# Performance work log

Hardware: AMD Instinct MI355X
Metric: run time of the kernel (lower is better)

Reference implementation:

```python
import jax, jax.numpy as jnp
import numpy as np

ND, NC = 100000, 20000
E_DD, E_DC, E_CD = 1600000, 800000, 800000
DDIM, CDIM, H, B = 256, 512, 128, 100000


def _lin_init(k, out_d, in_d):
    kw, kb = jax.random.split(k)
    s = 1.0 / np.sqrt(in_d)
    return (jax.random.uniform(kw, (out_d, in_d), jnp.float32, -s, s),
            jax.random.uniform(kb, (out_d,), jnp.float32, -s, s))


def setup_inputs() -> dict:
    key = jax.random.key(0)
    ks = jax.random.split(key, 32)
    inp = {
        'x_drug': jax.random.normal(ks[0], (ND, DDIM), jnp.float32),
        'x_cell': jax.random.normal(ks[1], (NC, CDIM), jnp.float32),
        'ei_dd_src': jax.random.randint(ks[2], (E_DD,), 0, ND),
        'ei_dd_dst': jax.random.randint(ks[3], (E_DD,), 0, ND),
        'ei_dc_src': jax.random.randint(ks[4], (E_DC,), 0, ND),
        'ei_dc_dst': jax.random.randint(ks[5], (E_DC,), 0, NC),
        'ei_cd_src': jax.random.randint(ks[6], (E_CD,), 0, NC),
        'ei_cd_dst': jax.random.randint(ks[7], (E_CD,), 0, ND),
        'q_da': jax.random.randint(ks[8], (B,), 0, ND),
        'q_db': jax.random.randint(ks[9], (B,), 0, ND),
        'q_c': jax.random.randint(ks[10], (B,), 0, NC),
    }
    # input projections
    inp['wd'], inp['bd'] = _lin_init(ks[11], H, DDIM)
    inp['wc'], inp['bc'] = _lin_init(ks[12], H, CDIM)
    # per-edge-type SAGEConv params: lin_l (W+b, on aggregated neighbors), lin_r (W only, on root)
    i = 13
    for name in ['dd1', 'cd1', 'dc1', 'dd2', 'cd2', 'dc2']:
        wl, bl = _lin_init(ks[i], H, H)
        wr, _ = _lin_init(ks[i + 1], H, H)
        inp[name + '_wl'], inp[name + '_bl'], inp[name + '_wr'] = wl, bl, wr
        i += 2
    # MLP head
    inp['m1_w'], inp['m1_b'] = _lin_init(ks[i], H, 3 * H)
    inp['m2_w'], inp['m2_b'] = _lin_init(ks[i + 1], 1, H)
    return inp


def _sage(x_src, x_dst, src, dst, wl, bl, wr):
    # SAGEConv: mean-aggregate neighbor (src) features onto dst, then lin_l + lin_r(root)
    n_dst = x_dst.shape[0]
    agg = jax.ops.segment_sum(x_src[src], dst, num_segments=n_dst)  # [n_dst, H]
    cnt = jax.ops.segment_sum(jnp.ones(src.shape, x_src.dtype), dst, num_segments=n_dst)
    mean = agg / jnp.maximum(cnt, 1.0)[:, None]
    return mean @ wl.T + bl + x_dst @ wr.T


def reference(x_drug, x_cell, wd, bd, wc, bc,
              dd1_wl, dd1_bl, dd1_wr, cd1_wl, cd1_bl, cd1_wr, dc1_wl, dc1_bl, dc1_wr,
              dd2_wl, dd2_bl, dd2_wr, cd2_wl, cd2_bl, cd2_wr, dc2_wl, dc2_bl, dc2_wr,
              m1_w, m1_b, m2_w, m2_b,
              ei_dd_src, ei_dd_dst, ei_dc_src, ei_dc_dst, ei_cd_src, ei_cd_dst,
              q_da, q_db, q_c):
    xd = x_drug @ wd.T + bd  # [ND, H]
    xc = x_cell @ wc.T + bc  # [NC, H]
    # layer 1 (to_hetero: sum contributions per dst node type, then relu)
    hd = jax.nn.relu(_sage(xd, xd, ei_dd_src, ei_dd_dst, dd1_wl, dd1_bl, dd1_wr)
                     + _sage(xc, xd, ei_cd_src, ei_cd_dst, cd1_wl, cd1_bl, cd1_wr))
    hc = jax.nn.relu(_sage(xd, xc, ei_dc_src, ei_dc_dst, dc1_wl, dc1_bl, dc1_wr))
    # layer 2 (no activation)
    od = (_sage(hd, hd, ei_dd_src, ei_dd_dst, dd2_wl, dd2_bl, dd2_wr)
          + _sage(hc, hd, ei_cd_src, ei_cd_dst, cd2_wl, cd2_bl, cd2_wr))
    oc = _sage(hd, hc, ei_dc_src, ei_dc_dst, dc2_wl, dc2_bl, dc2_wr)
    combined = jnp.concatenate([od[q_da], od[q_db], oc[q_c]], axis=-1)  # [B, 3H]
    h = jax.nn.relu(combined @ m1_w.T + m1_b)  # dropout is eval-mode identity
    return (h @ m2_w.T + m2_b)[:, 0]
```

## Files before the change

kernel.cpp:

```cpp
#include <hip/hip_runtime.h>
#include <hip/hip_fp16.h>

typedef _Float16 f16;
typedef f16 f16x8 __attribute__((ext_vector_type(8)));
typedef float f32x4 __attribute__((ext_vector_type(4)));

#define NDRUG 100000
#define NCELL 20000
#define EDD   1600000
#define EDC   800000
#define ECD   800000
#define NQ    100000
#define ETOT  (EDD + ECD + EDC)
#define CAP_DD 64
#define CAP_CD 64
#define CAP_DC 128

#define NBD 782
#define NBC 313
#define NBTOT (NBD + NBC)
#define ECHUNK 4096
#define NBLK ((ETOT + ECHUNK - 1) / ECHUNK)
#define BCAP 6144

__device__ inline int bucket_of(int rdst) { return rdst < 200000 ? (rdst >> 8) : NBD + ((rdst - 200000) >> 6); }
__device__ inline int dl_of(int rdst)     { return rdst < 200000 ? (rdst & 255) : ((rdst - 200000) & 63); }

__device__ inline int rdst_decode(int e, const int* __restrict__ ddd,
                                  const int* __restrict__ cdd, const int* __restrict__ dcd)
{
    if (e < EDD) return ddd[e];
    if (e < EDD + ECD) return 100000 + cdd[e - EDD];
    return 200000 + dcd[e - EDD - ECD];
}


__global__ __launch_bounds__(256) void hist_k(const int* __restrict__ ddd, const int* __restrict__ cdd,
                                              const int* __restrict__ dcd, int* __restrict__ bucket_tot)
{
    __shared__ int lh[NBTOT];
    for (int i = threadIdx.x; i < NBTOT; i += 256) lh[i] = 0;
    __syncthreads();
    int base = blockIdx.x * ECHUNK;
    for (int j = threadIdx.x; j < ECHUNK; j += 256) {
        int e = base + j;
        if (e < ETOT) atomicAdd(&lh[bucket_of(rdst_decode(e, ddd, cdd, dcd))], 1);
    }
    __syncthreads();
    for (int i = threadIdx.x; i < NBTOT; i += 256) {
        int c = lh[i];
        if (c) atomicAdd(&bucket_tot[i], c);
    }
}


__global__ __launch_bounds__(256) void scanbase_k(const int* __restrict__ tot,
                                                  int* __restrict__ basearr, int* __restrict__ cur)
{
    __shared__ int vals[1280];
    __shared__ int seg[256];
    int tid = threadIdx.x;
    for (int i = tid; i < 1280; i += 256) vals[i] = (i < NBTOT) ? tot[i] : 0;
    __syncthreads();
    int mine[5]; int s = 0;
#pragma unroll
    for (int j = 0; j < 5; ++j) { mine[j] = vals[tid * 5 + j]; s += mine[j]; }
    seg[tid] = s; __syncthreads();
    for (int o = 1; o < 256; o <<= 1) {
        int v = (tid >= o) ? seg[tid - o] : 0;
        __syncthreads();
        seg[tid] += v;
        __syncthreads();
    }
    int base = seg[tid] - s;
#pragma unroll
    for (int j = 0; j < 5; ++j) {
        int idx = tid * 5 + j;
        if (idx < NBTOT) { basearr[idx] = base; cur[idx] = base; }
        base += mine[j];
    }
}


__global__ __launch_bounds__(256) void scatter_k(
    const int* __restrict__ dds, const int* __restrict__ ddd,
    const int* __restrict__ cds, const int* __restrict__ cdd,
    const int* __restrict__ dcs, const int* __restrict__ dcd,
    int* __restrict__ bucket_cur, unsigned* __restrict__ binned)
{
    __shared__ int lh[NBTOT];
    __shared__ int lbase[NBTOT];
    __shared__ unsigned lrec[ECHUNK];
    __shared__ unsigned short lbkt[ECHUNK];
    for (int i = threadIdx.x; i < NBTOT; i += 256) lh[i] = 0;
    __syncthreads();
    int base = blockIdx.x * ECHUNK;
    for (int j = threadIdx.x; j < ECHUNK; j += 256) {
        int e = base + j;
        if (e < ETOT) {
            int src, rdst;
            if (e < EDD) { src = dds[e]; rdst = ddd[e]; }
            else if (e < EDD + ECD) { int i2 = e - EDD; src = cds[i2]; rdst = 100000 + cdd[i2]; }
            else { int i2 = e - EDD - ECD; src = dcs[i2]; rdst = 200000 + dcd[i2]; }
            int b = bucket_of(rdst);
            lrec[j] = ((unsigned)dl_of(rdst) << 17) | (unsigned)src;
            lbkt[j] = (unsigned short)b;
            atomicAdd(&lh[b], 1);
        } else {
            lbkt[j] = 0xFFFFu;
        }
    }
    __syncthreads();
    for (int i = threadIdx.x; i < NBTOT; i += 256) {
        int c = lh[i];
        lbase[i] = c ? atomicAdd(&bucket_cur[i], c) : 0;
        lh[i] = 0;
    }
    __syncthreads();
    for (int j = threadIdx.x; j < ECHUNK; j += 256) {
        unsigned short b = lbkt[j];
        if (b != 0xFFFFu) {
            int r = atomicAdd(&lh[b], 1);
            binned[lbase[b] + r] = lrec[j];
        }
    }
}


__global__ __launch_bounds__(256) void bucket_build_k(
    const unsigned* __restrict__ binned, const int* __restrict__ bucket_base, const int* __restrict__ bucket_tot,
    int* __restrict__ cnt_dd, int* __restrict__ cnt_cd, int* __restrict__ cnt_dc,
    int* __restrict__ l_dd, int* __restrict__ l_cd, int* __restrict__ l_dc)
{
    __shared__ unsigned recs[BCAP];
    __shared__ int cnt[256];
    __shared__ int off[256];
    __shared__ int cur[256];
    __shared__ int seg[256];

    int b = blockIdx.x, tid = threadIdx.x;
    int tot = bucket_tot[b];
    int base = bucket_base[b];
    int n = tot < BCAP ? tot : BCAP;

    cnt[tid] = 0;
    __syncthreads();
    for (int j = tid; j < n; j += 256) {
        unsigned r = binned[base + j];
        recs[j] = r;
        atomicAdd(&cnt[r >> 17], 1);
    }
    __syncthreads();
    int c = cnt[tid];
    seg[tid] = c; __syncthreads();
    for (int o = 1; o < 256; o <<= 1) {
        int v = (tid >= o) ? seg[tid - o] : 0;
        __syncthreads();
        seg[tid] += v;
        __syncthreads();
    }
    int ex = seg[tid] - c;
    off[tid] = ex; cur[tid] = ex;
    __syncthreads();

    for (int j = tid; j < n; j += 256) {
        unsigned r = recs[j];
        int dl = r >> 17;
        int src = r & 0x1FFFF;
        int rank = atomicAdd(&cur[dl], 1) - off[dl];
        if (b < NBD) {
            int rdst = b * 256 + dl;
            if (rdst < 100000) { if (rank < CAP_DD) l_dd[(size_t)rdst * CAP_DD + rank] = src; }
            else               { if (rank < CAP_CD) l_cd[(size_t)(rdst - 100000) * CAP_CD + rank] = src; }
        } else {
            int node = (b - NBD) * 64 + dl;
            if (rank < CAP_DC) l_dc[(size_t)node * CAP_DC + rank] = src;
        }
    }

    if (b < NBD) {
        int rdst = b * 256 + tid;
        if (rdst < 200000) {
            if (rdst < 100000) cnt_dd[rdst] = cnt[tid];
            else               cnt_cd[rdst - 100000] = cnt[tid];
        }
    } else {
        if (tid < 64) {
            int node = (b - NBD) * 64 + tid;
            if (node < NCELL) cnt_dc[node] = cnt[tid];
        }
    }
}


__device__ inline void addv(float* acc, uint4 v)
{
    const __half2* h = (const __half2*)&v;
#pragma unroll
    for (int j = 0; j < 4; ++j) {
        float2 f = __half22float2(h[j]);
        acc[2 * j]     += f.x;
        acc[2 * j + 1] += f.y;
    }
}

__global__ __launch_bounds__(256) void agg_all_k(
    const __half* __restrict__ t_d, const __half* __restrict__ t_c,
    const int* __restrict__ cnt_dd, const int* __restrict__ cnt_cd, const int* __restrict__ cnt_dc,
    const int* __restrict__ l_dd, const int* __restrict__ l_cd, const int* __restrict__ l_dc,
    __half* __restrict__ m_a, __half* __restrict__ m_b, __half* __restrict__ m_c)
{
    int node = blockIdx.x * 16 + (threadIdx.x >> 4);
    int g = threadIdx.x & 15;

    const int* list; int n; const __half* tab; __half* out;
    if (node < NDRUG) {
        list = l_dd + (size_t)node * CAP_DD; n = cnt_dd[node];
        if (n > CAP_DD) n = CAP_DD;
        tab = t_d; out = m_a + (size_t)node * 128;
    } else if (node < 2 * NDRUG) {
        int m = node - NDRUG;
        list = l_cd + (size_t)m * CAP_CD; n = cnt_cd[m];
        if (n > CAP_CD) n = CAP_CD;
        tab = t_c; out = m_b + (size_t)m * 128;
    } else if (node < 2 * NDRUG + NCELL) {
        int m = node - 2 * NDRUG;
        list = l_dc + (size_t)m * CAP_DC; n = cnt_dc[m];
        if (n > CAP_DC) n = CAP_DC;
        tab = t_d; out = m_c + (size_t)m * 128;
    } else return;

    const __half* base = tab + (size_t)g * 8;

    float acc[8];
#pragma unroll
    for (int j = 0; j < 8; ++j) acc[j] = 0.f;

    int i = 0;
    for (; i + 3 < n; i += 4) {
        int s0 = list[i], s1 = list[i + 1], s2 = list[i + 2], s3 = list[i + 3];
        uint4 v0 = *(const uint4*)(base + (size_t)s0 * 128);
        uint4 v1 = *(const uint4*)(base + (size_t)s1 * 128);
        uint4 v2 = *(const uint4*)(base + (size_t)s2 * 128);
        uint4 v3 = *(const uint4*)(base + (size_t)s3 * 128);
        addv(acc, v0); addv(acc, v1); addv(acc, v2); addv(acc, v3);
    }
    for (; i < n; ++i) {
        uint4 v = *(const uint4*)(base + (size_t)list[i] * 128);
        addv(acc, v);
    }

    float inv = 1.f / fmaxf((float)n, 1.f);
    __half h[8];
#pragma unroll
    for (int j = 0; j < 8; ++j) h[j] = __float2half(acc[j] * inv);
    *(uint4*)(out + g * 8) = *(uint4*)h;
}


__global__ __launch_bounds__(256) void prep_k(
    const float* __restrict__ wd,     const float* __restrict__ wc,     const float* __restrict__ m1w,
    const float* __restrict__ dd1_wl, const float* __restrict__ cd1_wl, const float* __restrict__ dc1_wl,
    const float* __restrict__ dc1_wr, const float* __restrict__ dd1_wr, const float* __restrict__ cd1_wr,
    const float* __restrict__ dd1_bl, const float* __restrict__ cd1_bl,
    const float* __restrict__ dd2_wl, const float* __restrict__ cd2_wl, const float* __restrict__ dc2_wl,
    const float* __restrict__ dc2_wr, const float* __restrict__ dd2_wr, const float* __restrict__ cd2_wr,
    const float* __restrict__ dd2_bl, const float* __restrict__ cd2_bl,
    f16* __restrict__ wd16, f16* __restrict__ wc16, f16* __restrict__ m1w16,
    f16* __restrict__ dd1_wl16, f16* __restrict__ cd1_wl16, f16* __restrict__ dc1_wl16,
    f16* __restrict__ dc1_wr16, f16* __restrict__ wr1s16,
    f16* __restrict__ dd2_wl16, f16* __restrict__ cd2_wl16, f16* __restrict__ dc2_wl16,
    f16* __restrict__ dc2_wr16, f16* __restrict__ wr2s16,
    float* __restrict__ bsum1, float* __restrict__ bsum2)
{
    int i = blockIdx.x * 256 + threadIdx.x;
    if (i < 128 * 256) wd16[i] = (f16)wd[i];
    if (i < 128 * 512) wc16[i] = (f16)wc[i];
    if (i < 128 * 384) m1w16[i] = (f16)m1w[i];
    if (i < 128 * 128) {
        dd1_wl16[i] = (f16)dd1_wl[i];
        cd1_wl16[i] = (f16)cd1_wl[i];
        dc1_wl16[i] = (f16)dc1_wl[i];
        dc1_wr16[i] = (f16)dc1_wr[i];
        wr1s16[i]   = (f16)(dd1_wr[i] + cd1_wr[i]);
        dd2_wl16[i] = (f16)dd2_wl[i];
        cd2_wl16[i] = (f16)cd2_wl[i];
        dc2_wl16[i] = (f16)dc2_wl[i];
        dc2_wr16[i] = (f16)dc2_wr[i];
        wr2s16[i]   = (f16)(dd2_wr[i] + cd2_wr[i]);
    }
    if (i < 128) {
        bsum1[i] = dd1_bl[i] + cd1_bl[i];
        bsum2[i] = dd2_bl[i] + cd2_bl[i];
    }
}


template<typename AT, int MODE>
__global__ __launch_bounds__(256) void mgemm_k(
    const AT* __restrict__ A0, const int* __restrict__ I0, const f16* __restrict__ W0, int K0, int S0,
    const AT* __restrict__ A1, const int* __restrict__ I1, const f16* __restrict__ W1, int K1, int S1,
    const AT* __restrict__ A2, const int* __restrict__ I2, const f16* __restrict__ W2, int K2, int S2,
    const float* __restrict__ bias, const float* __restrict__ m2w, const float* __restrict__ m2b,
    f16* __restrict__ Ch, float* __restrict__ Cf, int M)
{
    __shared__ f16 As[128][72];
    __shared__ f16 Ws[128][72];

    const int tid = threadIdx.x;
    const int w  = tid >> 6;
    const int l  = tid & 63;
    const int lc = l & 15;
    const int lq = l >> 4;
    const int mb = blockIdx.x * 128;
    const int sr = tid >> 1;
    const int sk = (tid & 1) * 32;

    f32x4 acc[2][8];
#pragma unroll
    for (int mi = 0; mi < 2; ++mi)
#pragma unroll
        for (int j = 0; j < 8; ++j) acc[mi][j] = (f32x4){0.f, 0.f, 0.f, 0.f};

    const AT*  Aseg[3] = {A0, A1, A2};
    const int* Iseg[3] = {I0, I1, I2};
    const f16* Wseg[3] = {W0, W1, W2};
    const int  Kseg[3] = {K0, K1, K2};
    const int  Sseg[3] = {S0, S1, S2};

    for (int s = 0; s < 3; ++s) {
        const AT* A = Aseg[s];
        if (!A) continue;
        const int* idx = Iseg[s];
        const f16* W = Wseg[s];
        const int K = Kseg[s], S = Sseg[s];

        int m = mb + sr; if (m >= M) m = M - 1;
        const AT*  arow = A + (size_t)(idx ? idx[m] : m) * (size_t)K;
        const f16* wrow = W + (size_t)sr * (size_t)S;

        for (int kt = 0; kt < K; kt += 64) {
            if constexpr (sizeof(AT) == 2) {
                const uint4* ap = (const uint4*)(arow + kt + sk);
                uint4 a0 = ap[0], a1 = ap[1], a2 = ap[2], a3 = ap[3];
                *(uint4*)&As[sr][sk]      = a0;
                *(uint4*)&As[sr][sk + 8]  = a1;
                *(uint4*)&As[sr][sk + 16] = a2;
                *(uint4*)&As[sr][sk + 24] = a3;
            } else {
                const float4* ap = (const float4*)(arow + kt + sk);
#pragma unroll
                for (int i = 0; i < 4; ++i) {
                    float4 u = ap[2 * i], v = ap[2 * i + 1];
                    f16x8 h;
                    h[0] = (f16)u.x; h[1] = (f16)u.y; h[2] = (f16)u.z; h[3] = (f16)u.w;
                    h[4] = (f16)v.x; h[5] = (f16)v.y; h[6] = (f16)v.z; h[7] = (f16)v.w;
                    *(f16x8*)&As[sr][sk + 8 * i] = h;
                }
            }
            {
                const uint4* wp = (const uint4*)(wrow + kt + sk);
                uint4 w0 = wp[0], w1 = wp[1], w2 = wp[2], w3 = wp[3];
                *(uint4*)&Ws[sr][sk]      = w0;
                *(uint4*)&Ws[sr][sk + 8]  = w1;
                *(uint4*)&Ws[sr][sk + 16] = w2;
                *(uint4*)&Ws[sr][sk + 24] = w3;
            }
            __syncthreads();

#pragma unroll
            for (int ks = 0; ks < 64; ks += 32) {
                f16x8 a0 = *(const f16x8*)&As[32 * w + lc][ks + 8 * lq];
                f16x8 a1 = *(const f16x8*)&As[32 * w + 16 + lc][ks + 8 * lq];
#pragma unroll
                for (int j = 0; j < 8; ++j) {
                    f16x8 b = *(const f16x8*)&Ws[16 * j + lc][ks + 8 * lq];
                    acc[0][j] = __builtin_amdgcn_mfma_f32_16x16x32_f16(a0, b, acc[0][j], 0, 0, 0);
                    acc[1][j] = __builtin_amdgcn_mfma_f32_16x16x32_f16(a1, b, acc[1][j], 0, 0, 0);
                }
            }
            __syncthreads();
        }
    }

    if (MODE == 2) {
        float part[2][4];
#pragma unroll
        for (int mi = 0; mi < 2; ++mi)
#pragma unroll
            for (int r = 0; r < 4; ++r) part[mi][r] = 0.f;
#pragma unroll
        for (int j = 0; j < 8; ++j) {
            float bj = bias[16 * j + lc];
            float wv = m2w[16 * j + lc];
#pragma unroll
            for (int mi = 0; mi < 2; ++mi)
#pragma unroll
                for (int r = 0; r < 4; ++r) {
                    float v = acc[mi][j][r] + bj;
                    v = v > 0.f ? v : 0.f;
                    part[mi][r] = fmaf(v, wv, part[mi][r]);
                }
        }
#pragma unroll
        for (int mi = 0; mi < 2; ++mi)
#pragma unroll
            for (int r = 0; r < 4; ++r) {
                float p = part[mi][r];
#pragma unroll
                for (int o = 1; o < 16; o <<= 1) p += __shfl_xor(p, o, 16);
                if (lc == 0) {
                    int row = mb + 32 * w + 16 * mi + 4 * lq + r;
                    if (row < M) Cf[row] = p + m2b[0];
                }
            }
    } else {
#pragma unroll
        for (int j = 0; j < 8; ++j) {
            float bj = bias[16 * j + lc];
#pragma unroll
            for (int mi = 0; mi < 2; ++mi)
#pragma unroll
                for (int r = 0; r < 4; ++r) {
                    float v = acc[mi][j][r] + bj;
                    if (MODE == 1) v = v > 0.f ? v : 0.f;
                    int row = mb + 32 * w + 16 * mi + 4 * lq + r;
                    if (row < M) Ch[(size_t)row * 128 + 16 * j + lc] = (f16)v;
                }
        }
    }
}


extern "C" void kernel_launch(void* const* d_in, const int* in_sizes, int n_in,
                              void* d_out, int out_size, void* d_ws, size_t ws_size,
                              hipStream_t stream)
{
    const float* x_drug = (const float*)d_in[0];
    const float* x_cell = (const float*)d_in[1];
    const int* ei_dd_src = (const int*)d_in[2];
    const int* ei_dd_dst = (const int*)d_in[3];
    const int* ei_dc_src = (const int*)d_in[4];
    const int* ei_dc_dst = (const int*)d_in[5];
    const int* ei_cd_src = (const int*)d_in[6];
    const int* ei_cd_dst = (const int*)d_in[7];
    const int* q_da = (const int*)d_in[8];
    const int* q_db = (const int*)d_in[9];
    const int* q_c  = (const int*)d_in[10];
    const float* wd = (const float*)d_in[11];
    const float* bd = (const float*)d_in[12];
    const float* wc = (const float*)d_in[13];
    const float* bc = (const float*)d_in[14];
    const float* dd1_wl = (const float*)d_in[15]; const float* dd1_bl = (const float*)d_in[16]; const float* dd1_wr = (const float*)d_in[17];
    const float* cd1_wl = (const float*)d_in[18]; const float* cd1_bl = (const float*)d_in[19]; const float* cd1_wr = (const float*)d_in[20];
    const float* dc1_wl = (const float*)d_in[21]; const float* dc1_bl = (const float*)d_in[22]; const float* dc1_wr = (const float*)d_in[23];
    const float* dd2_wl = (const float*)d_in[24]; const float* dd2_bl = (const float*)d_in[25]; const float* dd2_wr = (const float*)d_in[26];
    const float* cd2_wl = (const float*)d_in[27]; const float* cd2_bl = (const float*)d_in[28]; const float* cd2_wr = (const float*)d_in[29];
    const float* dc2_wl = (const float*)d_in[30]; const float* dc2_bl = (const float*)d_in[31]; const float* dc2_wr = (const float*)d_in[32];
    const float* m1_w = (const float*)d_in[33]; const float* m1_b = (const float*)d_in[34];
    const float* m2_w = (const float*)d_in[35]; const float* m2_b = (const float*)d_in[36];
    float* out = (float*)d_out;

    char* wsp = (char*)d_ws;
    size_t off = 0;
    auto alloc = [&](size_t bytes) -> void* {
        void* p = wsp + off;
        off += (bytes + 255) & ~(size_t)255;
        return p;
    };

    __half* xd_h     = (__half*)alloc((size_t)NDRUG * 128 * 2);
    __half* xc_h     = (__half*)alloc((size_t)NCELL * 128 * 2);
    __half* hd_h     = (__half*)alloc((size_t)NDRUG * 128 * 2);
    __half* hc_h     = (__half*)alloc((size_t)NCELL * 128 * 2);
    __half* mean_a_h = (__half*)alloc((size_t)NDRUG * 128 * 2);
    __half* mean_b_h = (__half*)alloc((size_t)NDRUG * 128 * 2);
    __half* mean_c_h = (__half*)alloc((size_t)NCELL * 128 * 2);
    __half* od_h     = (__half*)alloc((size_t)NDRUG * 128 * 2);
    __half* oc_h     = (__half*)alloc((size_t)NCELL * 128 * 2);

    f16* wd16     = (f16*)alloc(128 * 256 * 2);
    f16* wc16     = (f16*)alloc(128 * 512 * 2);
    f16* m1w16    = (f16*)alloc(128 * 384 * 2);
    f16* dd1_wl16 = (f16*)alloc(128 * 128 * 2);
    f16* cd1_wl16 = (f16*)alloc(128 * 128 * 2);
    f16* dc1_wl16 = (f16*)alloc(128 * 128 * 2);
    f16* dc1_wr16 = (f16*)alloc(128 * 128 * 2);
    f16* wr1s16   = (f16*)alloc(128 * 128 * 2);
    f16* dd2_wl16 = (f16*)alloc(128 * 128 * 2);
    f16* cd2_wl16 = (f16*)alloc(128 * 128 * 2);
    f16* dc2_wl16 = (f16*)alloc(128 * 128 * 2);
    f16* dc2_wr16 = (f16*)alloc(128 * 128 * 2);
    f16* wr2s16   = (f16*)alloc(128 * 128 * 2);
    float* bsum1  = (float*)alloc(128 * 4);
    float* bsum2  = (float*)alloc(128 * 4);

    int* cnt      = (int*)alloc((size_t)(2 * NDRUG + NCELL) * 4);
    int* cnt_dd   = cnt;
    int* cnt_cd   = cnt + NDRUG;
    int* cnt_dc   = cnt + 2 * NDRUG;
    int* l_dd     = (int*)alloc((size_t)NDRUG * CAP_DD * 4);
    int* l_cd     = (int*)alloc((size_t)NDRUG * CAP_CD * 4);
    int* l_dc     = (int*)alloc((size_t)NCELL * CAP_DC * 4);

    int* bucket_tot  = (int*)alloc((size_t)NBTOT * 4);
    int* bucket_base = (int*)alloc((size_t)NBTOT * 4);
    int* bucket_cur  = (int*)alloc((size_t)NBTOT * 4);
    unsigned* binned = (unsigned*)alloc((size_t)ETOT * 4);

    hipMemsetAsync(bucket_tot, 0, (size_t)NBTOT * 4, stream);
    hist_k<<<NBLK, 256, 0, stream>>>(ei_dd_dst, ei_cd_dst, ei_dc_dst, bucket_tot);
    scanbase_k<<<1, 256, 0, stream>>>(bucket_tot, bucket_base, bucket_cur);
    scatter_k<<<NBLK, 256, 0, stream>>>(ei_dd_src, ei_dd_dst, ei_cd_src, ei_cd_dst,
                                        ei_dc_src, ei_dc_dst, bucket_cur, binned);
    bucket_build_k<<<NBTOT, 256, 0, stream>>>(binned, bucket_base, bucket_tot,
                                              cnt_dd, cnt_cd, cnt_dc, l_dd, l_cd, l_dc);

    prep_k<<<256, 256, 0, stream>>>(
        wd, wc, m1_w,
        dd1_wl, cd1_wl, dc1_wl, dc1_wr, dd1_wr, cd1_wr, dd1_bl, cd1_bl,
        dd2_wl, cd2_wl, dc2_wl, dc2_wr, dd2_wr, cd2_wr, dd2_bl, cd2_bl,
        wd16, wc16, m1w16,
        dd1_wl16, cd1_wl16, dc1_wl16, dc1_wr16, wr1s16,
        dd2_wl16, cd2_wl16, dc2_wl16, dc2_wr16, wr2s16,
        bsum1, bsum2);

    const f16*   fnull = nullptr;
    const float* f32null = nullptr;
    const int*   inull = nullptr;
    const int GD = (NDRUG + 127) / 128;
    const int GC = (NCELL + 127) / 128;
    const int GQ = (NQ + 127) / 128;

    mgemm_k<float, 0><<<GD, 256, 0, stream>>>(
        x_drug, inull, wd16, 256, 256,
        f32null, inull, fnull, 0, 0,
        f32null, inull, fnull, 0, 0,
        bd, f32null, f32null, (f16*)xd_h, nullptr, NDRUG);
    mgemm_k<float, 0><<<GC, 256, 0, stream>>>(
        x_cell, inull, wc16, 512, 512,
        f32null, inull, fnull, 0, 0,
        f32null, inull, fnull, 0, 0,
        bc, f32null, f32null, (f16*)xc_h, nullptr, NCELL);

    const int AGG_GRID = (2 * NDRUG + NCELL + 15) / 16;

    agg_all_k<<<AGG_GRID, 256, 0, stream>>>(xd_h, xc_h, cnt_dd, cnt_cd, cnt_dc,
                                            l_dd, l_cd, l_dc, mean_a_h, mean_b_h, mean_c_h);

    mgemm_k<f16, 1><<<GD, 256, 0, stream>>>(
        (const f16*)mean_a_h, inull, dd1_wl16, 128, 128,
        (const f16*)mean_b_h, inull, cd1_wl16, 128, 128,
        (const f16*)xd_h,     inull, wr1s16,   128, 128,
        bsum1, f32null, f32null, (f16*)hd_h, nullptr, NDRUG);
    mgemm_k<f16, 1><<<GC, 256, 0, stream>>>(
        (const f16*)mean_c_h, inull, dc1_wl16, 128, 128,
        (const f16*)xc_h,     inull, dc1_wr16, 128, 128,
        fnull,                inull, fnull,    0, 0,
        dc1_bl, f32null, f32null, (f16*)hc_h, nullptr, NCELL);

    agg_all_k<<<AGG_GRID, 256, 0, stream>>>(hd_h, hc_h, cnt_dd, cnt_cd, cnt_dc,
                                            l_dd, l_cd, l_dc, mean_a_h, mean_b_h, mean_c_h);

    mgemm_k<f16, 0><<<GD, 256, 0, stream>>>(
        (const f16*)mean_a_h, inull, dd2_wl16, 128, 128,
        (const f16*)mean_b_h, inull, cd2_wl16, 128, 128,
        (const f16*)hd_h,     inull, wr2s16,   128, 128,
        bsum2, f32null, f32null, (f16*)od_h, nullptr, NDRUG);
    mgemm_k<f16, 0><<<GC, 256, 0, stream>>>(
        (const f16*)mean_c_h, inull, dc2_wl16, 128, 128,
        (const f16*)hc_h,     inull, dc2_wr16, 128, 128,
        fnull,                inull, fnull,    0, 0,
        dc2_bl, f32null, f32null, (f16*)oc_h, nullptr, NCELL);

    mgemm_k<f16, 2><<<GQ, 256, 0, stream>>>(
        (const f16*)od_h, q_da, m1w16,       128, 384,
        (const f16*)od_h, q_db, m1w16 + 128, 128, 384,
        (const f16*)oc_h, q_c,  m1w16 + 256, 128, 384,
        m1_b, m2_w, m2_b, nullptr, out, NQ);
}
```

Before: 530.4 us.

## Replace histogram+scan binning with fixed-capacity buckets and local-sorted scatter

Removes the separate histogram and global scan passes by giving each destination bucket a fixed-capacity slot region in the binned buffer, so scatter only needs an atomic cursor per bucket. Scatter now sorts each chunk's records by bucket in shared memory before writing, making global writes contiguous. Bucket build becomes a deterministic counting sort in shared memory, and the neighbor gather loop is unrolled to eight loads in flight. The risk is silent truncation if any bucket exceeds its fixed capacity, plus a larger binned buffer and higher shared memory use in scatter.

```diff
diff --git a/kernel.cpp b/kernel.cpp
--- a/kernel.cpp
+++ b/kernel.cpp
@@ -21,64 +21,17 @@
 #define NBTOT (NBD + NBC)
 #define ECHUNK 4096
 #define NBLK ((ETOT + ECHUNK - 1) / ECHUNK)
-#define BCAP 6144
+#define BCAP 8192
+#define LCAP 6144
 
 __device__ inline int bucket_of(int rdst) { return rdst < 200000 ? (rdst >> 8) : NBD + ((rdst - 200000) >> 6); }
 __device__ inline int dl_of(int rdst)     { return rdst < 200000 ? (rdst & 255) : ((rdst - 200000) & 63); }
 
-__device__ inline int rdst_decode(int e, const int* __restrict__ ddd,
-                                  const int* __restrict__ cdd, const int* __restrict__ dcd)
-{
-    if (e < EDD) return ddd[e];
-    if (e < EDD + ECD) return 100000 + cdd[e - EDD];
-    return 200000 + dcd[e - EDD - ECD];
-}
-
-
-__global__ __launch_bounds__(256) void hist_k(const int* __restrict__ ddd, const int* __restrict__ cdd,
-                                              const int* __restrict__ dcd, int* __restrict__ bucket_tot)
-{
-    __shared__ int lh[NBTOT];
-    for (int i = threadIdx.x; i < NBTOT; i += 256) lh[i] = 0;
-    __syncthreads();
-    int base = blockIdx.x * ECHUNK;
-    for (int j = threadIdx.x; j < ECHUNK; j += 256) {
-        int e = base + j;
-        if (e < ETOT) atomicAdd(&lh[bucket_of(rdst_decode(e, ddd, cdd, dcd))], 1);
-    }
-    __syncthreads();
-    for (int i = threadIdx.x; i < NBTOT; i += 256) {
-        int c = lh[i];
-        if (c) atomicAdd(&bucket_tot[i], c);
-    }
-}
-
-
-__global__ __launch_bounds__(256) void scanbase_k(const int* __restrict__ tot,
-                                                  int* __restrict__ basearr, int* __restrict__ cur)
-{
-    __shared__ int vals[1280];
-    __shared__ int seg[256];
-    int tid = threadIdx.x;
-    for (int i = tid; i < 1280; i += 256) vals[i] = (i < NBTOT) ? tot[i] : 0;
-    __syncthreads();
-    int mine[5]; int s = 0;
-#pragma unroll
-    for (int j = 0; j < 5; ++j) { mine[j] = vals[tid * 5 + j]; s += mine[j]; }
-    seg[tid] = s; __syncthreads();
-    for (int o = 1; o < 256; o <<= 1) {
-        int v = (tid >= o) ? seg[tid - o] : 0;
-        __syncthreads();
-        seg[tid] += v;
-        __syncthreads();
-    }
-    int base = seg[tid] - s;
-#pragma unroll
-    for (int j = 0; j < 5; ++j) {
-        int idx = tid * 5 + j;
-        if (idx < NBTOT) { basearr[idx] = base; cur[idx] = base; }
-        base += mine[j];
-    }
+
+__global__ void initcur_k(int* __restrict__ cur)
+{
+    int i = blockIdx.x * 256 + threadIdx.x;
+    if (i < NBTOT) cur[i] = i * BCAP;
 }
 
 
@@ -88,14 +41,23 @@
     const int* __restrict__ dcs, const int* __restrict__ dcd,
     int* __restrict__ bucket_cur, unsigned* __restrict__ binned)
 {
-    __shared__ int lh[NBTOT];
-    __shared__ int lbase[NBTOT];
     __shared__ unsigned lrec[ECHUNK];
     __shared__ unsigned short lbkt[ECHUNK];
-    for (int i = threadIdx.x; i < NBTOT; i += 256) lh[i] = 0;
-    __syncthreads();
+    __shared__ unsigned short lrank[ECHUNK];
+    __shared__ unsigned srec[ECHUNK];
+    __shared__ unsigned short sbkt[ECHUNK];
+    __shared__ int lh[NBTOT];
+    __shared__ int loff[NBTOT];
+    __shared__ int lbase[NBTOT];
+    __shared__ int seg[256];
+    __shared__ int nvalid_sh;
+
+    int tid = threadIdx.x;
+    for (int i = tid; i < NBTOT; i += 256) lh[i] = 0;
+    __syncthreads();
+
     int base = blockIdx.x * ECHUNK;
-    for (int j = threadIdx.x; j < ECHUNK; j += 256) {
+    for (int j = tid; j < ECHUNK; j += 256) {
         int e = base + j;
         if (e < ETOT) {
             int src, rdst;
@@ -105,50 +67,75 @@
             int b = bucket_of(rdst);
             lrec[j] = ((unsigned)dl_of(rdst) << 17) | (unsigned)src;
             lbkt[j] = (unsigned short)b;
-            atomicAdd(&lh[b], 1);
+            lrank[j] = (unsigned short)atomicAdd(&lh[b], 1);
         } else {
             lbkt[j] = 0xFFFFu;
         }
     }
     __syncthreads();
-    for (int i = threadIdx.x; i < NBTOT; i += 256) {
-        int c = lh[i];
-        lbase[i] = c ? atomicAdd(&bucket_cur[i], c) : 0;
-        lh[i] = 0;
-    }
-    __syncthreads();
-    for (int j = threadIdx.x; j < ECHUNK; j += 256) {
-        unsigned short b = lbkt[j];
-        if (b != 0xFFFFu) {
-            int r = atomicAdd(&lh[b], 1);
-            binned[lbase[b] + r] = lrec[j];
-        }
+
+    int mine[5], s = 0;
+#pragma unroll
+    for (int q = 0; q < 5; ++q) { int idx = tid * 5 + q; mine[q] = (idx < NBTOT) ? lh[idx] : 0; s += mine[q]; }
+    seg[tid] = s; __syncthreads();
+    for (int o = 1; o < 256; o <<= 1) {
+        int v = (tid >= o) ? seg[tid - o] : 0;
+        __syncthreads();
+        seg[tid] += v;
+        __syncthreads();
+    }
+    if (tid == 255) nvalid_sh = seg[255];
+    int run = seg[tid] - s;
+#pragma unroll
+    for (int q = 0; q < 5; ++q) {
+        int idx = tid * 5 + q;
+        if (idx < NBTOT) {
+            loff[idx] = run;
+            lbase[idx] = mine[q] ? atomicAdd(&bucket_cur[idx], mine[q]) : 0;
+        }
+        run += mine[q];
+    }
+    __syncthreads();
+
+    for (int j = tid; j < ECHUNK; j += 256) {
+        int b = lbkt[j];
+        if (b != 0xFFFF) {
+            int p = loff[b] + lrank[j];
+            srec[p] = lrec[j];
+            sbkt[p] = (unsigned short)b;
+        }
+    }
+    __syncthreads();
+
+    int nvalid = nvalid_sh;
+    for (int p = tid; p < nvalid; p += 256) {
+        int b = sbkt[p];
+        binned[lbase[b] + (p - loff[b])] = srec[p];
     }
 }
 
 
 __global__ __launch_bounds__(256) void bucket_build_k(
-    const unsigned* __restrict__ binned, const int* __restrict__ bucket_base, const int* __restrict__ bucket_tot,
+    const unsigned* __restrict__ binned, const int* __restrict__ bucket_cur,
     int* __restrict__ cnt_dd, int* __restrict__ cnt_cd, int* __restrict__ cnt_dc,
     int* __restrict__ l_dd, int* __restrict__ l_cd, int* __restrict__ l_dc)
 {
-    __shared__ unsigned recs[BCAP];
     __shared__ int cnt[256];
     __shared__ int off[256];
-    __shared__ int cur[256];
     __shared__ int seg[256];
+    __shared__ unsigned short lrank[LCAP];
+    __shared__ unsigned srec[LCAP];
 
     int b = blockIdx.x, tid = threadIdx.x;
-    int tot = bucket_tot[b];
-    int base = bucket_base[b];
-    int n = tot < BCAP ? tot : BCAP;
+    int gbase = b * BCAP;
+    int n = bucket_cur[b] - gbase;
+    n = n < 0 ? 0 : (n > LCAP ? LCAP : n);
 
     cnt[tid] = 0;
     __syncthreads();
     for (int j = tid; j < n; j += 256) {
-        unsigned r = binned[base + j];
-        recs[j] = r;
-        atomicAdd(&cnt[r >> 17], 1);
+        unsigned r = binned[gbase + j];
+        lrank[j] = (unsigned short)atomicAdd(&cnt[r >> 17], 1);
     }
     __syncthreads();
     int c = cnt[tid];
@@ -159,15 +146,21 @@
         seg[tid] += v;
         __syncthreads();
     }
-    int ex = seg[tid] - c;
-    off[tid] = ex; cur[tid] = ex;
+    off[tid] = seg[tid] - c;
     __syncthreads();
 
     for (int j = tid; j < n; j += 256) {
-        unsigned r = recs[j];
+        unsigned r = binned[gbase + j];
+        int p = off[r >> 17] + lrank[j];
+        srec[p] = r;
+    }
+    __syncthreads();
+
+    for (int p = tid; p < n; p += 256) {
+        unsigned r = srec[p];
         int dl = r >> 17;
+        int rank = p - off[dl];
         int src = r & 0x1FFFF;
-        int rank = atomicAdd(&cur[dl], 1) - off[dl];
         if (b < NBD) {
             int rdst = b * 256 + dl;
             if (rdst < 100000) { if (rank < CAP_DD) l_dd[(size_t)rdst * CAP_DD + rank] = src; }
@@ -237,12 +230,18 @@
     for (int j = 0; j < 8; ++j) acc[j] = 0.f;
 
     int i = 0;
+    for (; i + 7 < n; i += 8) {
+        uint4 v[8];
+#pragma unroll
+        for (int u = 0; u < 8; ++u) v[u] = *(const uint4*)(base + (size_t)list[i + u] * 128);
+#pragma unroll
+        for (int u = 0; u < 8; ++u) addv(acc, v[u]);
+    }
     for (; i + 3 < n; i += 4) {
-        int s0 = list[i], s1 = list[i + 1], s2 = list[i + 2], s3 = list[i + 3];
-        uint4 v0 = *(const uint4*)(base + (size_t)s0 * 128);
-        uint4 v1 = *(const uint4*)(base + (size_t)s1 * 128);
-        uint4 v2 = *(const uint4*)(base + (size_t)s2 * 128);
-        uint4 v3 = *(const uint4*)(base + (size_t)s3 * 128);
+        uint4 v0 = *(const uint4*)(base + (size_t)list[i] * 128);
+        uint4 v1 = *(const uint4*)(base + (size_t)list[i + 1] * 128);
+        uint4 v2 = *(const uint4*)(base + (size_t)list[i + 2] * 128);
+        uint4 v3 = *(const uint4*)(base + (size_t)list[i + 3] * 128);
         addv(acc, v0); addv(acc, v1); addv(acc, v2); addv(acc, v3);
     }
     for (; i < n; ++i) {
@@ -503,17 +502,13 @@
     int* l_cd     = (int*)alloc((size_t)NDRUG * CAP_CD * 4);
     int* l_dc     = (int*)alloc((size_t)NCELL * CAP_DC * 4);
 
-    int* bucket_tot  = (int*)alloc((size_t)NBTOT * 4);
-    int* bucket_base = (int*)alloc((size_t)NBTOT * 4);
     int* bucket_cur  = (int*)alloc((size_t)NBTOT * 4);
-    unsigned* binned = (unsigned*)alloc((size_t)ETOT * 4);
-
-    hipMemsetAsync(bucket_tot, 0, (size_t)NBTOT * 4, stream);
-    hist_k<<<NBLK, 256, 0, stream>>>(ei_dd_dst, ei_cd_dst, ei_dc_dst, bucket_tot);
-    scanbase_k<<<1, 256, 0, stream>>>(bucket_tot, bucket_base, bucket_cur);
+    unsigned* binned = (unsigned*)alloc((size_t)NBTOT * BCAP * 4);
+
+    initcur_k<<<(NBTOT + 255) / 256, 256, 0, stream>>>(bucket_cur);
     scatter_k<<<NBLK, 256, 0, stream>>>(ei_dd_src, ei_dd_dst, ei_cd_src, ei_cd_dst,
                                         ei_dc_src, ei_dc_dst, bucket_cur, binned);
-    bucket_build_k<<<NBTOT, 256, 0, stream>>>(binned, bucket_base, bucket_tot,
+    bucket_build_k<<<NBTOT, 256, 0, stream>>>(binned, bucket_cur,
                                               cnt_dd, cnt_cd, cnt_dc, l_dd, l_cd, l_dc);
 
     prep_k<<<256, 256, 0, stream>>>(
```

Result: slower. 553.9 us (+4.4%).
